# Kernel optimization log

Measured on AMD Instinct MI355X. Metric: run time of the kernel, lower is better.

The kernel has to match this reference:

```python
import jax, jax.numpy as jnp
import numpy as np

N_USER = 100_000
N_WALLET = 100_000
E = 1_600_000
HID, OUT = 128, 64
H, C = 4, 32  # GAT heads, per-head channels (HID // 4)
U_IN, W_IN = 16, 4
EPS = 1e-5


def _sage(x_src, x_dst, ei, w_l, b_l, w_r):
    """PyG SAGEConv (mean aggr): lin_l(mean_j x_j) + lin_r(x_i)."""
    src, dst = ei[0], ei[1]
    n = x_dst.shape[0]
    s = jax.ops.segment_sum(x_src[src], dst, num_segments=n)
    deg = jax.ops.segment_sum(jnp.ones((src.shape[0],), x_src.dtype), dst, num_segments=n)
    agg = s / jnp.maximum(deg, 1.0)[:, None]
    return agg @ w_l + b_l + x_dst @ w_r


def _bn(x, g, b):
    """BatchNorm over node dim (training-mode batch stats)."""
    m = x.mean(0)
    v = x.var(0)
    return (x - m) * jax.lax.rsqrt(v + EPS) * g + b


def _segment_softmax(logits, seg, n):
    m = jax.ops.segment_max(logits, seg, num_segments=n)
    e = jnp.exp(logits - m[seg])
    s = jax.ops.segment_sum(e, seg, num_segments=n)
    return e / (s[seg] + 1e-16)


def _gat(x, ei, w, a_src, a_dst, bias):
    """PyG GATConv with self-loops, heads concatenated. Dropout off (eval)."""
    n = x.shape[0]
    loop = jnp.arange(n, dtype=ei.dtype)
    src = jnp.concatenate([ei[0], loop])
    dst = jnp.concatenate([ei[1], loop])
    xp = (x @ w).reshape(n, H, C)                      # [n,H,C]
    al_s = (xp * a_src).sum(-1)                        # [n,H]
    al_d = (xp * a_dst).sum(-1)                        # [n,H]
    logits = jax.nn.leaky_relu(al_s[src] + al_d[dst], 0.2)  # [E+n,H]
    alpha = _segment_softmax(logits, dst, n)
    out = jax.ops.segment_sum(xp[src] * alpha[:, :, None], dst, num_segments=n)
    return out.reshape(n, H * C) + bias


def setup_inputs() -> dict:
    key = jax.random.key(0)
    ks = jax.random.split(key, 24)
    rn = lambda k, s, sc=0.05: jax.random.normal(k, s, jnp.float32) * sc
    ei = lambda k, n: jax.random.randint(k, (2, E), 0, n, jnp.int32)
    return {
        "x_user": rn(ks[0], (N_USER, U_IN), 1.0),
        "x_wallet": rn(ks[1], (N_WALLET, W_IN), 1.0),
        "w_u2w_l": rn(ks[2], (U_IN, HID)), "b_u2w": jnp.zeros((HID,), jnp.float32), "w_u2w_r": rn(ks[3], (W_IN, HID)),
        "w_w2u_l": rn(ks[4], (W_IN, HID)), "b_w2u": jnp.zeros((HID,), jnp.float32), "w_w2u_r": rn(ks[5], (U_IN, HID)),
        "w_u2u_l": rn(ks[6], (U_IN, HID)), "b_u2u": jnp.zeros((HID,), jnp.float32), "w_u2u_r": rn(ks[7], (U_IN, HID)),
        "bn_u_g": jnp.ones((HID,), jnp.float32), "bn_u_b": jnp.zeros((HID,), jnp.float32),
        "bn_w_g": jnp.ones((HID,), jnp.float32), "bn_w_b": jnp.zeros((HID,), jnp.float32),
        "gat_w": rn(ks[8], (HID, H * C)), "gat_as": rn(ks[9], (H, C)), "gat_ad": rn(ks[10], (H, C)),
        "gat_b": jnp.zeros((HID,), jnp.float32),
        "bn2_g": jnp.ones((HID,), jnp.float32), "bn2_b": jnp.zeros((HID,), jnp.float32),
        "proj_w": rn(ks[11], (HID, OUT)), "proj_b": jnp.zeros((OUT,), jnp.float32),
        "ei_uw": ei(ks[12], N_USER),   # src user -> dst wallet (both 100k)
        "ei_wu": ei(ks[13], N_WALLET),  # src wallet -> dst user
        "ei_uu": ei(ks[14], N_USER),
    }


def reference(x_user, x_wallet, w_u2w_l, b_u2w, w_u2w_r, w_w2u_l, b_w2u, w_w2u_r,
              w_u2u_l, b_u2u, w_u2u_r, bn_u_g, bn_u_b, bn_w_g, bn_w_b,
              gat_w, gat_as, gat_ad, gat_b, bn2_g, bn2_b, proj_w, proj_b,
              ei_uw, ei_wu, ei_uu):
    h_w_from_u = jax.nn.relu(_sage(x_user, x_wallet, ei_uw, w_u2w_l, b_u2w, w_u2w_r))
    h_u_from_w = jax.nn.relu(_sage(x_wallet, x_user, ei_wu, w_w2u_l, b_w2u, w_w2u_r))
    h_u_from_u = jax.nn.relu(_sage(x_user, x_user, ei_uu, w_u2u_l, b_u2u, w_u2u_r))
    h_user = _bn(h_u_from_w + h_u_from_u, bn_u_g, bn_u_b)
    _ = _bn(h_w_from_u, bn_w_g, bn_w_b)  # h_wallet: computed in torch module but unused in output
    h_user = jax.nn.relu(_gat(h_user, ei_uu, gat_w, gat_as, gat_ad, gat_b))
    h_user = _bn(h_user, bn2_g, bn2_b)
    return jax.nn.relu(h_user @ proj_w + proj_b)  # dropout = identity (eval)
```

## Files before the change

### kernel.cpp

```cpp
#include <hip/hip_runtime.h>
#include <hip/hip_bf16.h>
#include <cstdint>
#include <cstddef>

#define NN   100000
#define NE   1600000
#define CAP  48

#define NBKT 784
#define BSH  7
#define FB   8
#define BCAP 2432
#define ACHUNK 2048
#define NABLK 784

#define NTILES 1563
#define CH_BN 500
#define LOG2E 1.44269504088896f

typedef __attribute__((ext_vector_type(8))) short short8;
typedef __attribute__((ext_vector_type(4))) float floatx4;

__device__ inline short f2bs(float x) {
    __hip_bfloat16 h = __float2bfloat16(x);
    return *reinterpret_cast<short*>(&h);
}
__device__ inline int pack2(float a, float b) {
    return ((int)(unsigned short)f2bs(b) << 16) | (unsigned short)f2bs(a);
}
__device__ inline float bflo(unsigned p) { return __uint_as_float(p << 16); }
__device__ inline float bfhi(unsigned p) { return __uint_as_float(p & 0xFFFF0000u); }

#define OFF_PRE   ((size_t)0)
#define OFF_BKTU  ((size_t)0)
#define OFF_BKTW  ((size_t)1906688)
#define OFF_XP    ((size_t)12800000)
#define OFF_AGGU  ((size_t)12800000)
#define OFF_AGGW  ((size_t)14400000)
#define OFF_COLU  ((size_t)19200000)
#define OFF_CNTU  ((size_t)25600000)
#define OFF_BCUR  ((size_t)25800000)
#define OFF_S1    ((size_t)25801600)
#define OFF_Q1    ((size_t)25801728)
#define OFF_S2    ((size_t)25801856)
#define OFF_Q2    ((size_t)25801984)
#define OFF_ALS   ((size_t)25802112)
#define OFF_ALD   ((size_t)26202112)
#define ZBASE     OFF_BCUR
#define ZFLOATS   ((size_t)2112)

__global__ void __launch_bounds__(256) bin_edges(
    const int* __restrict__ ei_u, const int* __restrict__ ei_w,
    int* __restrict__ bcur_u, int* __restrict__ bkt_u,
    int* __restrict__ bcur_w, int* __restrict__ bkt_w) {
    const int* ei = blockIdx.y ? ei_w : ei_u;
    int* bcur = blockIdx.y ? bcur_w : bcur_u;
    int* bkt  = blockIdx.y ? bkt_w  : bkt_u;
    __shared__ int lcnt[NBKT];
    __shared__ int lbuf[NBKT * FB];
    for (int i = threadIdx.x; i < NBKT; i += 256) lcnt[i] = 0;
    __syncthreads();
    int base = blockIdx.x * ACHUNK;
    #pragma unroll
    for (int k = 0; k < ACHUNK / 256; k++) {
        int e = base + k * 256 + threadIdx.x;
        if (e < NE) {
            int src = ei[e], dst = ei[NE + e];
            int b = dst >> BSH;
            int pk = ((dst & ((1 << BSH) - 1)) << 17) | src;
            int pos = atomicAdd(&lcnt[b], 1);
            if (pos < FB) lbuf[b * FB + pos] = pk;
            else {
                int g = atomicAdd(&bcur[b], 1);
                if (g < BCAP) bkt[(size_t)b * BCAP + g] = pk;
            }
        }
    }
    __syncthreads();
    int wid = threadIdx.x >> 6, lane = threadIdx.x & 63;
    const int BPW = NBKT / 4;
    int b0w = wid * BPW;
    for (int r = 0; r < BPW; r += 64) {
        int rb = r + lane;
        if (rb < BPW) {
            int b = b0w + rb;
            int c = lcnt[b];
            int nn2 = c < FB ? c : FB;
            if (nn2 > 0) {
                int g0 = atomicAdd(&bcur[b], nn2);
                for (int i2 = 0; i2 < nn2; i2++) {
                    int g = g0 + i2;
                    if (g < BCAP) bkt[(size_t)b * BCAP + g] = lbuf[b * FB + i2];
                }
            }
        }
    }
}

__global__ void __launch_bounds__(256) csr_agg(
    const int* __restrict__ bcur_u, const int* __restrict__ bkt_u,
    int* __restrict__ cnt_g, int* __restrict__ col_g,
    const float* __restrict__ xu, float* __restrict__ aggu,
    const int* __restrict__ bcur_w, const int* __restrict__ bkt_w,
    const float* __restrict__ xw, float* __restrict__ aggw) {
    int type = blockIdx.y;
    const int* bcur = type ? bcur_w : bcur_u;
    const int* bkt  = type ? bkt_w  : bkt_u;
    int B = blockIdx.x;
    int node_base = B << BSH;
    if (node_base >= NN) return;
    __shared__ int cnt[128];
    __shared__ int col[128 * CAP];
    if (threadIdx.x < 128) cnt[threadIdx.x] = 0;
    __syncthreads();
    int n = bcur[B]; if (n > BCAP) n = BCAP;
    const int* bp = bkt + (size_t)B * BCAP;
    for (int i = threadIdx.x; i < n; i += 256) {
        int p = bp[i];
        int d = p >> 17;
        int pos = atomicAdd(&cnt[d], 1);
        if (pos < CAP) col[d * CAP + pos] = p & 0x1FFFF;
    }
    __syncthreads();
    int nn_here = NN - node_base; if (nn_here > 128) nn_here = 128;
    int wv = threadIdx.x >> 6, lane = threadIdx.x & 63;

    if (type == 0) {
        if (threadIdx.x < nn_here) cnt_g[node_base + threadIdx.x] = cnt[threadIdx.x];
        int total4 = nn_here * CAP / 4;
        const int4* cs = (const int4*)col;
        int4* cg = (int4*)(col_g + (size_t)node_base * CAP);
        for (int i = threadIdx.x; i < total4; i += 256) cg[i] = cs[i];
        int j = lane >> 4, k = lane & 15;
        for (int nl = wv * 32; nl < wv * 32 + 32 && nl < nn_here; nl++) {
            int deg = cnt[nl];
            int nu = deg < CAP ? deg : CAP;
            float v0 = 0.f, v1 = 0.f, v2 = 0.f, v3 = 0.f;
            int iters = (nu + 15) >> 4;
            for (int it = 0; it < iters; it++) {
                int bb = j + (it << 4);
                int s0 = (bb < nu)      ? col[nl * CAP + bb]      : 0;
                int s1 = (bb + 4 < nu)  ? col[nl * CAP + bb + 4]  : 0;
                int s2 = (bb + 8 < nu)  ? col[nl * CAP + bb + 8]  : 0;
                int s3 = (bb + 12 < nu) ? col[nl * CAP + bb + 12] : 0;
                float x0 = xu[(size_t)s0 * 16 + k];
                float x1 = xu[(size_t)s1 * 16 + k];
                float x2 = xu[(size_t)s2 * 16 + k];
                float x3 = xu[(size_t)s3 * 16 + k];
                if (bb < nu)      v0 += x0;
                if (bb + 4 < nu)  v1 += x1;
                if (bb + 8 < nu)  v2 += x2;
                if (bb + 12 < nu) v3 += x3;
            }
            float v = (v0 + v1) + (v2 + v3);
            v += __shfl_xor(v, 16, 64);
            v += __shfl_xor(v, 32, 64);
            if (lane < 16)
                aggu[(size_t)(node_base + nl) * 16 + lane] = v / fmaxf((float)deg, 1.f);
        }
    } else {
        int j = lane >> 2, k = lane & 3;
        for (int nl = wv * 32; nl < wv * 32 + 32 && nl < nn_here; nl++) {
            int deg = cnt[nl];
            int nw = deg < CAP ? deg : CAP;
            float v = 0.f;
            int iters = (nw + 15) >> 4;
            for (int it = 0; it < iters; it++) {
                int bb = j + (it << 4);
                int s = (bb < nw) ? col[nl * CAP + bb] : 0;
                float x = xw[(size_t)s * 4 + k];
                if (bb < nw) v += x;
            }
            v += __shfl_xor(v, 4, 64);
            v += __shfl_xor(v, 8, 64);
            v += __shfl_xor(v, 16, 64);
            v += __shfl_xor(v, 32, 64);
            if (lane < 4)
                aggw[(size_t)(node_base + nl) * 4 + lane] = v / fmaxf((float)deg, 1.f);
        }
    }
}

__global__ void __launch_bounds__(256, 2) sage_gemm(
    const float* __restrict__ aggu, const float* __restrict__ aggw,
    const float* __restrict__ xu,
    const float* __restrict__ wl_w2u, const float* __restrict__ b_w2u, const float* __restrict__ wr_w2u,
    const float* __restrict__ wl_u2u, const float* __restrict__ b_u2u, const float* __restrict__ wr_u2u,
    __hip_bfloat16* __restrict__ pre) {
    __shared__ short lw[16 * 64 * 8];
    __shared__ short la[64 * 136];
    int tid = threadIdx.x;
    for (int idx = tid; idx < 8192; idx += 256) {
        int mat = idx >> 12;
        int k = (idx >> 7) & 31, n = idx & 127;
        float w;
        if (mat == 0)
            w = (k < 4) ? wl_w2u[k * 128 + n] : (k < 20 ? wr_w2u[(k - 4) * 128 + n] : 0.f);
        else
            w = (k < 16) ? wl_u2u[k * 128 + n] : wr_u2u[(k - 16) * 128 + n];
        int t = n >> 4, l15 = n & 15, q = (k >> 3) & 3, j = k & 7;
        lw[((mat * 8 + t) * 64 + q * 16 + l15) * 8 + j] = f2bs(w);
    }
    __syncthreads();
    int wv = tid >> 6, lane = tid & 63;
    int quad = lane >> 4, l15 = lane & 15;
    short8 w1[8], w2[8];
    #pragma unroll
    for (int t = 0; t < 8; t++) {
        w1[t] = *(const short8*)&lw[(t * 64 + lane) * 8];
        w2[t] = *(const short8*)&lw[((8 + t) * 64 + lane) * 8];
    }
    float bw[8], bu[8];
    #pragma unroll
    for (int t = 0; t < 8; t++) {
        bw[t] = b_w2u[t * 16 + l15];
        bu[t] = b_u2u[t * 16 + l15];
    }
    for (int tile = blockIdx.x; tile < NTILES; tile += gridDim.x) {
        int nbase = tile * 64;
        __syncthreads();
        {
            int node = tid >> 2, p = tid & 3;
            int gn = nbase + node;
            float4 v = make_float4(0.f, 0.f, 0.f, 0.f);
            if (gn < NN) v = *(const float4*)&xu[(size_t)gn * 16 + 4 * p];
            int2 pk; pk.x = pack2(v.x, v.y); pk.y = pack2(v.z, v.w);
            *(int2*)&la[node * 136 + 4 + 4 * p] = pk;
            *(int2*)&la[node * 136 + 48 + 4 * p] = pk;
        }
        {
            int node = tid >> 2, p = tid & 3;
            int gn = nbase + node;
            float4 v = make_float4(0.f, 0.f, 0.f, 0.f);
            if (gn < NN) v = *(const float4*)&aggu[(size_t)gn * 16 + 4 * p];
            int2 pk; pk.x = pack2(v.x, v.y); pk.y = pack2(v.z, v.w);
            *(int2*)&la[node * 136 + 32 + 4 * p] = pk;
        }
        if (tid < 64) {
            int node = tid, gn = nbase + node;
            float4 v = make_float4(0.f, 0.f, 0.f, 0.f);
            if (gn < NN) v = *(const float4*)&aggw[(size_t)gn * 4];
            int2 pk; pk.x = pack2(v.x, v.y); pk.y = pack2(v.z, v.w);
            *(int2*)&la[node * 136 + 0] = pk;
            int2 z; z.x = 0; z.y = 0;
            *(int2*)&la[node * 136 + 20] = z;
            *(int2*)&la[node * 136 + 24] = z;
            *(int2*)&la[node * 136 + 28] = z;
        }
        __syncthreads();
        short8 af1 = *(const short8*)&la[(wv * 16 + l15) * 136 + quad * 8];
        short8 af2 = *(const short8*)&la[(wv * 16 + l15) * 136 + 32 + quad * 8];
        floatx4 acc1[8], acc2[8];
        #pragma unroll
        for (int t = 0; t < 8; t++) {
            acc1[t] = (floatx4){0.f, 0.f, 0.f, 0.f};
            acc2[t] = (floatx4){0.f, 0.f, 0.f, 0.f};
        }
        #pragma unroll
        for (int t = 0; t < 8; t++) {
            acc1[t] = __builtin_amdgcn_mfma_f32_16x16x32_bf16(af1, w1[t], acc1[t], 0, 0, 0);
            acc2[t] = __builtin_amdgcn_mfma_f32_16x16x32_bf16(af2, w2[t], acc2[t], 0, 0, 0);
        }
        __syncthreads();
        #pragma unroll
        for (int t = 0; t < 8; t++)
            #pragma unroll
            for (int r = 0; r < 4; r++) {
                float v1 = fmaxf(acc1[t][r] + bw[t], 0.f);
                float v2 = fmaxf(acc2[t][r] + bu[t], 0.f);
                la[(wv * 16 + quad * 4 + r) * 136 + t * 16 + l15] = f2bs(v1 + v2);
            }
        __syncthreads();
        #pragma unroll
        for (int c = 0; c < 4; c++) {
            int idx = c * 256 + tid;
            int node = idx >> 4, f8 = (idx & 15) * 8;
            int gn = nbase + node;
            if (gn < NN)
                *(int4*)(pre + (size_t)gn * 128 + f8) = *(const int4*)&la[node * 136 + f8];
        }
    }
}

__global__ void __launch_bounds__(256) bn_stats_pre2(const unsigned* __restrict__ x2,
                                                     float* __restrict__ sum, float* __restrict__ sq) {
    int f2 = threadIdx.x & 63, half = threadIdx.x >> 6;
    int n0 = blockIdx.x * CH_BN;
    float s0 = 0.f, q0 = 0.f, s1 = 0.f, q1 = 0.f;
    for (int i = n0 + half; i < n0 + CH_BN; i += 4) {
        unsigned p = x2[(size_t)i * 64 + f2];
        float v0 = bflo(p), v1 = bfhi(p);
        s0 += v0; q0 += v0 * v0; s1 += v1; q1 += v1 * v1;
    }
    __shared__ float a0[256], c0[256], a1[256], c1[256];
    a0[threadIdx.x] = s0; c0[threadIdx.x] = q0;
    a1[threadIdx.x] = s1; c1[threadIdx.x] = q1;
    __syncthreads();
    if (half == 0) {
        for (int h = 1; h < 4; h++) {
            s0 += a0[h * 64 + f2]; q0 += c0[h * 64 + f2];
            s1 += a1[h * 64 + f2]; q1 += c1[h * 64 + f2];
        }
        atomicAdd(&sum[2 * f2], s0);     atomicAdd(&sq[2 * f2], q0);
        atomicAdd(&sum[2 * f2 + 1], s1); atomicAdd(&sq[2 * f2 + 1], q1);
    }
}

__global__ void __launch_bounds__(256) bn_stats_act2(const unsigned* __restrict__ x2,
                                                     const float* __restrict__ gb,
                                                     float* __restrict__ sum, float* __restrict__ sq) {
    int f2 = threadIdx.x & 63, half = threadIdx.x >> 6;
    int n0 = blockIdx.x * CH_BN;
    float gb0 = gb[2 * f2], gb1 = gb[2 * f2 + 1];
    float s0 = 0.f, q0 = 0.f, s1 = 0.f, q1 = 0.f;
    for (int i = n0 + half; i < n0 + CH_BN; i += 4) {
        unsigned p = x2[(size_t)i * 64 + f2];
        float v0 = fmaxf(bflo(p) + gb0, 0.f), v1 = fmaxf(bfhi(p) + gb1, 0.f);
        s0 += v0; q0 += v0 * v0; s1 += v1; q1 += v1 * v1;
    }
    __shared__ float a0[256], c0[256], a1[256], c1[256];
    a0[threadIdx.x] = s0; c0[threadIdx.x] = q0;
    a1[threadIdx.x] = s1; c1[threadIdx.x] = q1;
    __syncthreads();
    if (half == 0) {
        for (int h = 1; h < 4; h++) {
            s0 += a0[h * 64 + f2]; q0 += c0[h * 64 + f2];
            s1 += a1[h * 64 + f2]; q1 += c1[h * 64 + f2];
        }
        atomicAdd(&sum[2 * f2], s0);     atomicAdd(&sq[2 * f2], q0);
        atomicAdd(&sum[2 * f2 + 1], s1); atomicAdd(&sq[2 * f2 + 1], q1);
    }
}

__global__ void __launch_bounds__(256, 2) gemm_al(
    const unsigned* __restrict__ pre2, const float* __restrict__ s1, const float* __restrict__ q1,
    const float* __restrict__ bng, const float* __restrict__ bnb,
    const float* __restrict__ gw, const float* __restrict__ gas, const float* __restrict__ gad,
    __hip_bfloat16* __restrict__ xp, float* __restrict__ al_s, float* __restrict__ al_d) {
    __shared__ short lw[32 * 64 * 8];
    __shared__ short la[64 * 136];
    __shared__ float lsc[128], lsh[128];
    int tid = threadIdx.x;
    if (tid < 128) {
        float m = s1[tid] * (1.0f / NN);
        float v = q1[tid] * (1.0f / NN) - m * m;
        float sc = bng[tid] * rsqrtf(v + 1e-5f);
        lsc[tid] = sc; lsh[tid] = bnb[tid] - m * sc;
    }
    for (int idx = tid; idx < 16384; idx += 256) {
        int k = idx >> 7, n = idx & 127;
        int t = n >> 4, l15 = n & 15, s = k >> 5, q = (k >> 3) & 3, j = k & 7;
        lw[(((t * 4 + s) * 64) + q * 16 + l15) * 8 + j] = f2bs(gw[idx]);
    }
    __syncthreads();
    int wv = tid >> 6, lane = tid & 63;
    int quad = lane >> 4, l15 = lane & 15;
    short8 wfrag[8][4];
    #pragma unroll
    for (int t = 0; t < 8; t++)
        #pragma unroll
        for (int s = 0; s < 4; s++)
            wfrag[t][s] = *(const short8*)&lw[((t * 4 + s) * 64 + lane) * 8];
    float asv[8], adv[8];
    #pragma unroll
    for (int t = 0; t < 8; t++) {
        asv[t] = gas[t * 16 + l15] * LOG2E;
        adv[t] = gad[t * 16 + l15] * LOG2E;
    }
    for (int tile = blockIdx.x; tile < NTILES; tile += gridDim.x) {
        int nbase = tile * 64;
        __syncthreads();
        #pragma unroll
        for (int c = 0; c < 8; c++) {
            int idx = c * 256 + tid;
            int node = idx >> 5, g = idx & 31;
            uint2 pp = make_uint2(0u, 0u);
            int gn = nbase + node;
            if (gn < NN) pp = *(const uint2*)&pre2[(size_t)gn * 64 + 2 * g];
            int f = 4 * g;
            float v0 = bflo(pp.x), v1 = bfhi(pp.x), v2 = bflo(pp.y), v3 = bfhi(pp.y);
            int2 pk;
            pk.x = pack2(v0 * lsc[f] + lsh[f],         v1 * lsc[f + 1] + lsh[f + 1]);
            pk.y = pack2(v2 * lsc[f + 2] + lsh[f + 2], v3 * lsc[f + 3] + lsh[f + 3]);
            *(int2*)&la[node * 136 + f] = pk;
        }
        __syncthreads();
        short8 af[4];
        #pragma unroll
        for (int s = 0; s < 4; s++)
            af[s] = *(const short8*)&la[(wv * 16 + l15) * 136 + s * 32 + quad * 8];
        floatx4 acc[8];
        #pragma unroll
        for (int t = 0; t < 8; t++) acc[t] = (floatx4){0.f, 0.f, 0.f, 0.f};
        #pragma unroll
        for (int s = 0; s < 4; s++)
            #pragma unroll
            for (int t = 0; t < 8; t++)
                acc[t] = __builtin_amdgcn_mfma_f32_16x16x32_bf16(af[s], wfrag[t][s], acc[t], 0, 0, 0);
        #pragma unroll
        for (int r = 0; r < 4; r++) {
            int node = nbase + wv * 16 + quad * 4 + r;
            #pragma unroll
            for (int h = 0; h < 4; h++) {
                float vs = acc[2 * h][r] * asv[2 * h] + acc[2 * h + 1][r] * asv[2 * h + 1];
                float vd = acc[2 * h][r] * adv[2 * h] + acc[2 * h + 1][r] * adv[2 * h + 1];
                #pragma unroll
                for (int m = 8; m >= 1; m >>= 1) {
                    vs += __shfl_xor(vs, m, 64);
                    vd += __shfl_xor(vd, m, 64);
                }
                if (l15 == 0 && node < NN) {
                    al_s[(size_t)node * 4 + h] = vs;
                    al_d[(size_t)node * 4 + h] = vd;
                }
            }
        }
        __syncthreads();
        #pragma unroll
        for (int t = 0; t < 8; t++)
            #pragma unroll
            for (int r = 0; r < 4; r++)
                la[(wv * 16 + quad * 4 + r) * 136 + t * 16 + l15] = f2bs(acc[t][r]);
        __syncthreads();
        #pragma unroll
        for (int c = 0; c < 4; c++) {
            int idx = c * 256 + tid;
            int node = idx >> 4, f8 = (idx & 15) * 8;
            int gn = nbase + node;
            if (gn < NN)
                *(int4*)(xp + (size_t)gn * 128 + f8) = *(const int4*)&la[node * 136 + f8];
        }
    }
}

__global__ void __launch_bounds__(256, 2) gemm_proj(
    const unsigned* __restrict__ gat2, const float* __restrict__ gb,
    const float* __restrict__ s2, const float* __restrict__ q2,
    const float* __restrict__ bng, const float* __restrict__ bnb,
    const float* __restrict__ pw, const float* __restrict__ pb,
    float* __restrict__ out) {
    __shared__ short lw[16 * 64 * 8];
    __shared__ short la[64 * 136];
    __shared__ float lsc[128], lsh[128], lgb[128];
    int tid = threadIdx.x;
    if (tid < 128) {
        float m = s2[tid] * (1.0f / NN);
        float v = q2[tid] * (1.0f / NN) - m * m;
        float sc = bng[tid] * rsqrtf(v + 1e-5f);
        lsc[tid] = sc; lsh[tid] = bnb[tid] - m * sc;
        lgb[tid] = gb[tid];
    }
    for (int idx = tid; idx < 8192; idx += 256) {
        int k = idx >> 6, n = idx & 63;
        int t = n >> 4, l15 = n & 15, s = k >> 5, q = (k >> 3) & 3, j = k & 7;
        lw[(((t * 4 + s) * 64) + q * 16 + l15) * 8 + j] = f2bs(pw[idx]);
    }
    __syncthreads();
    int wv = tid >> 6, lane = tid & 63;
    int quad = lane >> 4, l15 = lane & 15;
    short8 wfrag[4][4];
    #pragma unroll
    for (int t = 0; t < 4; t++)
        #pragma unroll
        for (int s = 0; s < 4; s++)
            wfrag[t][s] = *(const short8*)&lw[((t * 4 + s) * 64 + lane) * 8];
    float pbv[4];
    #pragma unroll
    for (int t = 0; t < 4; t++) pbv[t] = pb[t * 16 + l15];
    for (int tile = blockIdx.x; tile < NTILES; tile += gridDim.x) {
        int nbase = tile * 64;
        __syncthreads();
        #pragma unroll
        for (int c = 0; c < 8; c++) {
            int idx = c * 256 + tid;
            int node = idx >> 5, g = idx & 31;
            uint2 pp = make_uint2(0u, 0u);
            int gn = nbase + node;
            if (gn < NN) pp = *(const uint2*)&gat2[(size_t)gn * 64 + 2 * g];
            int f = 4 * g;
            float h0 = fmaxf(bflo(pp.x) + lgb[f],     0.f) * lsc[f]     + lsh[f];
            float h1 = fmaxf(bfhi(pp.x) + lgb[f + 1], 0.f) * lsc[f + 1] + lsh[f + 1];
            float h2 = fmaxf(bflo(pp.y) + lgb[f + 2], 0.f) * lsc[f + 2] + lsh[f + 2];
            float h3 = fmaxf(bfhi(pp.y) + lgb[f + 3], 0.f) * lsc[f + 3] + lsh[f + 3];
            int2 pk; pk.x = pack2(h0, h1); pk.y = pack2(h2, h3);
            *(int2*)&la[node * 136 + f] = pk;
        }
        __syncthreads();
        short8 af[4];
        #pragma unroll
        for (int s = 0; s < 4; s++)
            af[s] = *(const short8*)&la[(wv * 16 + l15) * 136 + s * 32 + quad * 8];
        floatx4 acc[4];
        #pragma unroll
        for (int t = 0; t < 4; t++) acc[t] = (floatx4){0.f, 0.f, 0.f, 0.f};
        #pragma unroll
        for (int s = 0; s < 4; s++)
            #pragma unroll
            for (int t = 0; t < 4; t++)
                acc[t] = __builtin_amdgcn_mfma_f32_16x16x32_bf16(af[s], wfrag[t][s], acc[t], 0, 0, 0);
        #pragma unroll
        for (int r = 0; r < 4; r++) {
            int gn = nbase + wv * 16 + quad * 4 + r;
            if (gn < NN) {
                #pragma unroll
                for (int t = 0; t < 4; t++)
                    out[(size_t)gn * 64 + t * 16 + l15] = fmaxf(acc[t][r] + pbv[t], 0.f);
            }
        }
    }
}

__global__ void __launch_bounds__(256) gat_gather(
    const int* __restrict__ cnt_u, const int* __restrict__ col_u,
    const float* __restrict__ al_s, const float* __restrict__ al_d,
    const unsigned* __restrict__ xp2, unsigned* __restrict__ gout2) {
    int i = (blockIdx.x * 256 + threadIdx.x) >> 6;
    int lane = threadIdx.x & 63;
    int h = lane >> 4;
    float ad = al_d[(size_t)i * 4 + h];
    int deg = cnt_u[i];
    int n = deg < CAP ? deg : CAP;
    int mycol = (lane < n) ? col_u[(size_t)i * CAP + lane] : 0;
    float l = al_s[(size_t)i * 4 + h] + ad;
    float e = exp2f(fmaxf(l, 0.2f * l));
    unsigned p = xp2[(size_t)i * 64 + lane];
    float acc0 = e * bflo(p), acc1 = e * bfhi(p), den = e;
    int b = 0;
    for (; b + 4 <= n; b += 4) {
        int s0 = __shfl(mycol, b, 64);
        int s1 = __shfl(mycol, b + 1, 64);
        int s2 = __shfl(mycol, b + 2, 64);
        int s3 = __shfl(mycol, b + 3, 64);
        float a0 = al_s[(size_t)s0 * 4 + h];
        float a1 = al_s[(size_t)s1 * 4 + h];
        float a2 = al_s[(size_t)s2 * 4 + h];
        float a3 = al_s[(size_t)s3 * 4 + h];
        unsigned p0 = xp2[(size_t)s0 * 64 + lane];
        unsigned p1 = xp2[(size_t)s1 * 64 + lane];
        unsigned p2 = xp2[(size_t)s2 * 64 + lane];
        unsigned p3 = xp2[(size_t)s3 * 64 + lane];
        float l0 = a0 + ad, l1 = a1 + ad, l2 = a2 + ad, l3 = a3 + ad;
        float e0 = exp2f(fmaxf(l0, 0.2f * l0));
        float e1 = exp2f(fmaxf(l1, 0.2f * l1));
        float e2 = exp2f(fmaxf(l2, 0.2f * l2));
        float e3 = exp2f(fmaxf(l3, 0.2f * l3));
        acc0 += e0 * bflo(p0) + e1 * bflo(p1) + e2 * bflo(p2) + e3 * bflo(p3);
        acc1 += e0 * bfhi(p0) + e1 * bfhi(p1) + e2 * bfhi(p2) + e3 * bfhi(p3);
        den  += e0 + e1 + e2 + e3;
    }
    for (; b < n; b++) {
        int s = __shfl(mycol, b, 64);
        float a = al_s[(size_t)s * 4 + h];
        unsigned pp = xp2[(size_t)s * 64 + lane];
        float ll = a + ad;
        float ee = exp2f(fmaxf(ll, 0.2f * ll));
        acc0 += ee * bflo(pp);
        acc1 += ee * bfhi(pp);
        den += ee;
    }
    float r = 1.0f / (den + 1e-16f);
    gout2[(size_t)i * 64 + lane] = (unsigned)pack2(acc0 * r, acc1 * r);
}

extern "C" void kernel_launch(void* const* d_in, const int* in_sizes, int n_in,
                              void* d_out, int out_size, void* d_ws, size_t ws_size,
                              hipStream_t stream) {
    const float* x_user   = (const float*)d_in[0];
    const float* x_wallet = (const float*)d_in[1];
    const float* w_w2u_l  = (const float*)d_in[5];
    const float* b_w2u    = (const float*)d_in[6];
    const float* w_w2u_r  = (const float*)d_in[7];
    const float* w_u2u_l  = (const float*)d_in[8];
    const float* b_u2u    = (const float*)d_in[9];
    const float* w_u2u_r  = (const float*)d_in[10];
    const float* bn_u_g   = (const float*)d_in[11];
    const float* bn_u_b   = (const float*)d_in[12];
    const float* gat_w    = (const float*)d_in[15];
    const float* gat_as   = (const float*)d_in[16];
    const float* gat_ad   = (const float*)d_in[17];
    const float* gat_b    = (const float*)d_in[18];
    const float* bn2_g    = (const float*)d_in[19];
    const float* bn2_b    = (const float*)d_in[20];
    const float* proj_w   = (const float*)d_in[21];
    const float* proj_b   = (const float*)d_in[22];
    const int* ei_wu      = (const int*)d_in[24];
    const int* ei_uu      = (const int*)d_in[25];
    float* out = (float*)d_out;
    float* ws  = (float*)d_ws;

    unsigned* pre2 = (unsigned*)(ws + OFF_PRE);
    __hip_bfloat16* pre = (__hip_bfloat16*)(ws + OFF_PRE);
    int*   bkt_u  = (int*)(ws + OFF_BKTU);
    int*   bkt_w  = (int*)(ws + OFF_BKTW);
    __hip_bfloat16* xp = (__hip_bfloat16*)(ws + OFF_XP);
    unsigned* xp2 = (unsigned*)(ws + OFF_XP);
    float* aggu = ws + OFF_AGGU;
    float* aggw = ws + OFF_AGGW;
    int*   col_u  = (int*)(ws + OFF_COLU);
    int*   cnt_u  = (int*)(ws + OFF_CNTU);
    int*   bcur_u = (int*)(ws + OFF_BCUR);
    int*   bcur_w = (int*)(ws + OFF_BCUR) + 800;
    float* al_s = ws + OFF_ALS, *al_d = ws + OFF_ALD;
    float* s1 = ws + OFF_S1, *q1 = ws + OFF_Q1;
    float* s2 = ws + OFF_S2, *q2 = ws + OFF_Q2;

    hipMemsetAsync(ws + ZBASE, 0, ZFLOATS * sizeof(float), stream);

    bin_edges<<<dim3(NABLK, 2), 256, 0, stream>>>(ei_uu, ei_wu, bcur_u, bkt_u, bcur_w, bkt_w);

    csr_agg<<<dim3(NBKT, 2), 256, 0, stream>>>(
        bcur_u, bkt_u, cnt_u, col_u, x_user, aggu,
        bcur_w, bkt_w, x_wallet, aggw);

    sage_gemm<<<512, 256, 0, stream>>>(
        aggu, aggw, x_user, w_w2u_l, b_w2u, w_w2u_r, w_u2u_l, b_u2u, w_u2u_r, pre);

    bn_stats_pre2<<<NN / CH_BN, 256, 0, stream>>>(pre2, s1, q1);

    gemm_al<<<512, 256, 0, stream>>>(pre2, s1, q1, bn_u_g, bn_u_b,
                                     gat_w, gat_as, gat_ad, xp, al_s, al_d);

    unsigned* gat2 = pre2;
    gat_gather<<<NN / 4, 256, 0, stream>>>(cnt_u, col_u, al_s, al_d, xp2, gat2);

    bn_stats_act2<<<NN / CH_BN, 256, 0, stream>>>(gat2, gat_b, s2, q2);

    gemm_proj<<<512, 256, 0, stream>>>(gat2, gat_b, s2, q2, bn2_g, bn2_b,
                                       proj_w, proj_b, out);
}
```

Measured before the change: 479.3 us.

## Split GAT gather wave into four neighbor groups with 16-byte row loads

The GAT gather kernel now splits each 64-lane wave into four 16-lane groups. Each group handles a different neighbor, and each lane loads a uint4 (8 bf16 values) of the source row instead of one 32-bit word. Partial sums are combined across groups with xor shuffles and written by the first group as a 16-byte store. This is meant to cut the number of serial loop iterations and use wider memory transactions. In exchange it adds a cross-group reduction, some masked wasted work on ragged degrees, and only a quarter of the lanes active for the store.

```diff
diff --git a/kernel.cpp b/kernel.cpp
--- a/kernel.cpp
+++ b/kernel.cpp
@@ -516,50 +516,54 @@
     const unsigned* __restrict__ xp2, unsigned* __restrict__ gout2) {
     int i = (blockIdx.x * 256 + threadIdx.x) >> 6;
     int lane = threadIdx.x & 63;
-    int h = lane >> 4;
+    int g = lane >> 4, q = lane & 15;
+    int h = q >> 2;
     float ad = al_d[(size_t)i * 4 + h];
     int deg = cnt_u[i];
     int n = deg < CAP ? deg : CAP;
     int mycol = (lane < n) ? col_u[(size_t)i * CAP + lane] : 0;
-    float l = al_s[(size_t)i * 4 + h] + ad;
-    float e = exp2f(fmaxf(l, 0.2f * l));
-    unsigned p = xp2[(size_t)i * 64 + lane];
-    float acc0 = e * bflo(p), acc1 = e * bfhi(p), den = e;
-    int b = 0;
-    for (; b + 4 <= n; b += 4) {
-        int s0 = __shfl(mycol, b, 64);
-        int s1 = __shfl(mycol, b + 1, 64);
-        int s2 = __shfl(mycol, b + 2, 64);
-        int s3 = __shfl(mycol, b + 3, 64);
-        float a0 = al_s[(size_t)s0 * 4 + h];
-        float a1 = al_s[(size_t)s1 * 4 + h];
-        float a2 = al_s[(size_t)s2 * 4 + h];
-        float a3 = al_s[(size_t)s3 * 4 + h];
-        unsigned p0 = xp2[(size_t)s0 * 64 + lane];
-        unsigned p1 = xp2[(size_t)s1 * 64 + lane];
-        unsigned p2 = xp2[(size_t)s2 * 64 + lane];
-        unsigned p3 = xp2[(size_t)s3 * 64 + lane];
-        float l0 = a0 + ad, l1 = a1 + ad, l2 = a2 + ad, l3 = a3 + ad;
-        float e0 = exp2f(fmaxf(l0, 0.2f * l0));
-        float e1 = exp2f(fmaxf(l1, 0.2f * l1));
-        float e2 = exp2f(fmaxf(l2, 0.2f * l2));
-        float e3 = exp2f(fmaxf(l3, 0.2f * l3));
-        acc0 += e0 * bflo(p0) + e1 * bflo(p1) + e2 * bflo(p2) + e3 * bflo(p3);
-        acc1 += e0 * bfhi(p0) + e1 * bfhi(p1) + e2 * bfhi(p2) + e3 * bfhi(p3);
-        den  += e0 + e1 + e2 + e3;
-    }
-    for (; b < n; b++) {
-        int s = __shfl(mycol, b, 64);
+    float a0 = 0.f, a1 = 0.f, a2 = 0.f, a3 = 0.f;
+    float a4 = 0.f, a5 = 0.f, a6 = 0.f, a7 = 0.f, den = 0.f;
+    if (g == 0) {
+        float l = al_s[(size_t)i * 4 + h] + ad;
+        float e = exp2f(fmaxf(l, 0.2f * l));
+        uint4 p = *(const uint4*)&xp2[(size_t)i * 64 + 4 * q];
+        a0 = e * bflo(p.x); a1 = e * bfhi(p.x);
+        a2 = e * bflo(p.y); a3 = e * bfhi(p.y);
+        a4 = e * bflo(p.z); a5 = e * bfhi(p.z);
+        a6 = e * bflo(p.w); a7 = e * bfhi(p.w);
+        den = e;
+    }
+    for (int b = 0; b < n; b += 4) {
+        int s = __shfl(mycol, b + g, 64);
         float a = al_s[(size_t)s * 4 + h];
-        unsigned pp = xp2[(size_t)s * 64 + lane];
-        float ll = a + ad;
-        float ee = exp2f(fmaxf(ll, 0.2f * ll));
-        acc0 += ee * bflo(pp);
-        acc1 += ee * bfhi(pp);
-        den += ee;
-    }
-    float r = 1.0f / (den + 1e-16f);
-    gout2[(size_t)i * 64 + lane] = (unsigned)pack2(acc0 * r, acc1 * r);
+        uint4 p = *(const uint4*)&xp2[(size_t)s * 64 + 4 * q];
+        float l = a + ad;
+        float e = (b + g < n) ? exp2f(fmaxf(l, 0.2f * l)) : 0.f;
+        a0 += e * bflo(p.x); a1 += e * bfhi(p.x);
+        a2 += e * bflo(p.y); a3 += e * bfhi(p.y);
+        a4 += e * bflo(p.z); a5 += e * bfhi(p.z);
+        a6 += e * bflo(p.w); a7 += e * bfhi(p.w);
+        den += e;
+    }
+    a0 += __shfl_xor(a0, 16, 64); a0 += __shfl_xor(a0, 32, 64);
+    a1 += __shfl_xor(a1, 16, 64); a1 += __shfl_xor(a1, 32, 64);
+    a2 += __shfl_xor(a2, 16, 64); a2 += __shfl_xor(a2, 32, 64);
+    a3 += __shfl_xor(a3, 16, 64); a3 += __shfl_xor(a3, 32, 64);
+    a4 += __shfl_xor(a4, 16, 64); a4 += __shfl_xor(a4, 32, 64);
+    a5 += __shfl_xor(a5, 16, 64); a5 += __shfl_xor(a5, 32, 64);
+    a6 += __shfl_xor(a6, 16, 64); a6 += __shfl_xor(a6, 32, 64);
+    a7 += __shfl_xor(a7, 16, 64); a7 += __shfl_xor(a7, 32, 64);
+    den += __shfl_xor(den, 16, 64); den += __shfl_xor(den, 32, 64);
+    if (g == 0) {
+        float r = 1.0f / (den + 1e-16f);
+        uint4 o;
+        o.x = (unsigned)pack2(a0 * r, a1 * r);
+        o.y = (unsigned)pack2(a2 * r, a3 * r);
+        o.z = (unsigned)pack2(a4 * r, a5 * r);
+        o.w = (unsigned)pack2(a6 * r, a7 * r);
+        *(uint4*)&gout2[(size_t)i * 64 + 4 * q] = o;
+    }
 }
 
 extern "C" void kernel_launch(void* const* d_in, const int* in_sizes, int n_in,
```

Measured after the change: 484.2 us. About the same (+1.0%).
